# Performance work log

Measured on AMD Instinct MI355X. Metric: run time of the kernel, lower is better.

Reference implementation:

```python
import jax, jax.numpy as jnp
import numpy as np

E, T, A, H = 64, 128, 32, 4
S, O, QH1, QD, C1 = 256, 128, 128, 64, 128  # state, obs, query hidden, query/key dim, c hidden


def setup_inputs() -> dict:
    key = jax.random.key(0)
    ks = jax.random.split(key, 10)
    w = 0.02
    return {
        "q_values": jax.random.normal(ks[0], (E, T, A), jnp.float32),
        "states": jax.random.normal(ks[1], (E, T, S), jnp.float32),
        "individual_fs": jax.random.normal(ks[2], (E, T, A, O), jnp.float32),
        "Wq1": jax.random.normal(ks[3], (S, QH1), jnp.float32) * w,
        "bq1": jnp.zeros((QH1,), jnp.float32),
        "Wq2": jax.random.normal(ks[4], (QH1, QD), jnp.float32) * w,
        "bq2": jnp.zeros((QD,), jnp.float32),
        "Wk": jax.random.normal(ks[5], (H, O, QD), jnp.float32) * w,
        "bk": jnp.zeros((H, QD), jnp.float32),
        "Wc1": jax.random.normal(ks[6], (S, C1), jnp.float32) * w,
        "bc1": jnp.zeros((C1,), jnp.float32),
        "Wc2": jax.random.normal(ks[7], (C1, 1), jnp.float32) * w,
        "bc2": jnp.zeros((1,), jnp.float32),
    }


def reference(q_values, states, individual_fs, Wq1, bq1, Wq2, bq2, Wk, bk, Wc1, bc1, Wc2, bc2):
    e, t, a = q_values.shape
    s = states.reshape(-1, states.shape[-1])              # (B, S), B = E*T
    f = individual_fs.reshape(e * t, a, -1)               # (B, A, O)
    # query embedding of state: 2-layer MLP with ReLU
    emb_s = jnp.maximum(s @ Wq1 + bq1, 0.0) @ Wq2 + bq2   # (B, QD)
    # all-agents, all-heads key extraction in one batched einsum
    emb_u = jnp.einsum('bao,hok->bahk', f, Wk) + bk       # (B, A, H, QD)
    # query-key dot products per agent/head, then sum over heads
    Lambda_i = jnp.einsum('bk,bahk->bah', emb_s, emb_u).sum(axis=-1)  # (B, A)
    # state-dependent scalar bias
    c_value = jnp.maximum(s @ Wc1 + bc1, 0.0) @ Wc2 + bc2  # (B, 1)
    Q_tot = jnp.sum(Lambda_i * q_values.reshape(-1, a), axis=-1, keepdims=True) + c_value
    return Q_tot.reshape(e, t, 1)
```

## Files before the change

### kernel.cpp

```cpp
#include <hip/hip_runtime.h>


static constexpr int Sd  = 256;
static constexpr int Ad  = 32;
static constexpr int Od  = 128;
static constexpr int QDd = 64;
static constexpr int NB  = 8;

__global__ void qatten_prep(const float* __restrict__ Wk, const float* __restrict__ bk,
                            float* __restrict__ WkT, float* __restrict__ bkSum)
{
    int idx = blockIdx.x * 256 + threadIdx.x;
    int k = idx >> 7;
    int o = idx & 127;
    float s = 0.f;
#pragma unroll
    for (int h = 0; h < 4; ++h) s += Wk[h * (Od * QDd) + o * QDd + k];
    WkT[k * Od + o] = s;
    if (idx < QDd) {
        float t = 0.f;
#pragma unroll
        for (int h = 0; h < 4; ++h) t += bk[h * QDd + idx];
        bkSum[idx] = t;
    }
}

__global__ __launch_bounds__(256, 4) void qatten_fused(
    const float* __restrict__ qv, const float* __restrict__ st, const float* __restrict__ fs,
    const float* __restrict__ Wq1, const float* __restrict__ bq1,
    const float* __restrict__ Wq2, const float* __restrict__ bq2,
    const float* __restrict__ Wc1, const float* __restrict__ bc1,
    const float* __restrict__ Wc2, const float* __restrict__ bc2,
    const float* __restrict__ WkT, const float* __restrict__ bkSum,
    float* __restrict__ out)
{
    __shared__ float s_lds[NB][Sd];
    __shared__ float h_lds[NB][260];
    __shared__ float emb_lds[NB][QDd];
    __shared__ float v_lds[NB][Od];
    __shared__ float q_lds[NB][Ad];
    __shared__ float red_lds[NB][4];
    __shared__ float bias_lds[NB];

    const int tid = threadIdx.x;
    const int b0 = blockIdx.x * NB;

    {
        const float4* sp = (const float4*)(st + (size_t)b0 * Sd);
        float4* sl = (float4*)&s_lds[0][0];
        sl[tid] = sp[tid];
        sl[tid + 256] = sp[tid + 256];
        (&q_lds[0][0])[tid] = qv[(size_t)b0 * Ad + tid];
    }
    __syncthreads();

    {
        const float* W  = (tid < 128) ? (Wq1 + tid) : (Wc1 + (tid - 128));
        const float  bb = (tid < 128) ? bq1[tid] : bc1[tid - 128];
        float acc[NB];
#pragma unroll
        for (int r = 0; r < NB; ++r) acc[r] = 0.f;
#pragma unroll 4
        for (int i = 0; i < Sd; i += 4) {
            const float w0 = W[(size_t)(i + 0) * 128];
            const float w1 = W[(size_t)(i + 1) * 128];
            const float w2 = W[(size_t)(i + 2) * 128];
            const float w3 = W[(size_t)(i + 3) * 128];
#pragma unroll
            for (int r = 0; r < NB; ++r) {
                const float4 sv = *(const float4*)&s_lds[r][i];
                float a = acc[r];
                a = fmaf(sv.x, w0, a);
                a = fmaf(sv.y, w1, a);
                a = fmaf(sv.z, w2, a);
                a = fmaf(sv.w, w3, a);
                acc[r] = a;
            }
        }
#pragma unroll
        for (int r = 0; r < NB; ++r)
            h_lds[r][tid] = fmaxf(acc[r] + bb, 0.f);
    }
    __syncthreads();

    {
        const int k = tid & 63;
        const int rg = tid >> 6;
        float a0 = 0.f, a1 = 0.f;
#pragma unroll 4
        for (int j = 0; j < 128; j += 4) {
            const float w0 = Wq2[(size_t)(j + 0) * 64 + k];
            const float w1 = Wq2[(size_t)(j + 1) * 64 + k];
            const float w2 = Wq2[(size_t)(j + 2) * 64 + k];
            const float w3 = Wq2[(size_t)(j + 3) * 64 + k];
            const float4 h0 = *(const float4*)&h_lds[rg][j];
            const float4 h1 = *(const float4*)&h_lds[rg + 4][j];
            a0 = fmaf(h0.x, w0, a0);  a1 = fmaf(h1.x, w0, a1);
            a0 = fmaf(h0.y, w1, a0);  a1 = fmaf(h1.y, w1, a1);
            a0 = fmaf(h0.z, w2, a0);  a1 = fmaf(h1.z, w2, a1);
            a0 = fmaf(h0.w, w3, a0);  a1 = fmaf(h1.w, w3, a1);
        }
        const float bias = bq2[k];
        emb_lds[rg][k] = a0 + bias;
        emb_lds[rg + 4][k] = a1 + bias;
    }
    __syncthreads();

    {
        const int o = tid & 127;
        const int rg = (tid >> 7) * 4;
        float acc[4] = {0.f, 0.f, 0.f, 0.f};
#pragma unroll 4
        for (int k = 0; k < QDd; k += 4) {
            const float w0 = WkT[(size_t)(k + 0) * 128 + o];
            const float w1 = WkT[(size_t)(k + 1) * 128 + o];
            const float w2 = WkT[(size_t)(k + 2) * 128 + o];
            const float w3 = WkT[(size_t)(k + 3) * 128 + o];
#pragma unroll
            for (int r = 0; r < 4; ++r) {
                const float4 ev = *(const float4*)&emb_lds[rg + r][k];
                float a = acc[r];
                a = fmaf(ev.x, w0, a);
                a = fmaf(ev.y, w1, a);
                a = fmaf(ev.z, w2, a);
                a = fmaf(ev.w, w3, a);
                acc[r] = a;
            }
        }
#pragma unroll
        for (int r = 0; r < 4; ++r) v_lds[rg + r][o] = acc[r];
    }

    {
        const int b = tid >> 5;
        const int i = tid & 31;
        float pb = 0.f, pc = 0.f;
#pragma unroll
        for (int k = i; k < QDd; k += 32)  pb = fmaf(emb_lds[b][k], bkSum[k], pb);
#pragma unroll
        for (int j = i; j < 128; j += 32)  pc = fmaf(h_lds[b][128 + j], Wc2[j], pc);
        float pq = q_lds[b][i];
#pragma unroll
        for (int d = 16; d >= 1; d >>= 1) {
            pb += __shfl_down(pb, d, 32);
            pc += __shfl_down(pc, d, 32);
            pq += __shfl_down(pq, d, 32);
        }
        if (i == 0) bias_lds[b] = (pc + bc2[0]) + pb * pq;
    }
    __syncthreads();

    {
        const int oq = tid & 31;
        const int ag = tid >> 5;
        float acc[NB];
#pragma unroll
        for (int b = 0; b < NB; ++b) {
            const float4* fb = (const float4*)(fs + (size_t)(b0 + b) * (Ad * Od));
            const float4 v4 = *(const float4*)&v_lds[b][oq * 4];
            float s = 0.f;
#pragma unroll
            for (int r = 0; r < 4; ++r) {
                const int a = ag + 8 * r;
                const float4 f4 = fb[a * 32 + oq];
                float d = f4.x * v4.x;
                d = fmaf(f4.y, v4.y, d);
                d = fmaf(f4.z, v4.z, d);
                d = fmaf(f4.w, v4.w, d);
                s = fmaf(q_lds[b][a], d, s);
            }
            acc[b] = s;
        }
        const int lane = tid & 63;
        const int wv = tid >> 6;
#pragma unroll
        for (int b = 0; b < NB; ++b) {
            float s = acc[b];
#pragma unroll
            for (int d = 32; d >= 1; d >>= 1) s += __shfl_xor(s, d);
            acc[b] = s;
        }
        if (lane == 0) {
#pragma unroll
            for (int b = 0; b < NB; ++b) red_lds[b][wv] = acc[b];
        }
    }
    __syncthreads();

    if (tid < NB) {
        out[b0 + tid] = red_lds[tid][0] + red_lds[tid][1] +
                        red_lds[tid][2] + red_lds[tid][3] + bias_lds[tid];
    }
}

extern "C" void kernel_launch(void* const* d_in, const int* in_sizes, int n_in,
                              void* d_out, int out_size, void* d_ws, size_t ws_size,
                              hipStream_t stream) {
    const float* qv  = (const float*)d_in[0];
    const float* st  = (const float*)d_in[1];
    const float* fs  = (const float*)d_in[2];
    const float* Wq1 = (const float*)d_in[3];
    const float* bq1 = (const float*)d_in[4];
    const float* Wq2 = (const float*)d_in[5];
    const float* bq2 = (const float*)d_in[6];
    const float* Wk  = (const float*)d_in[7];
    const float* bk  = (const float*)d_in[8];
    const float* Wc1 = (const float*)d_in[9];
    const float* bc1 = (const float*)d_in[10];
    const float* Wc2 = (const float*)d_in[11];
    const float* bc2 = (const float*)d_in[12];
    float* out = (float*)d_out;

    float* WkT   = (float*)d_ws;
    float* bkSum = WkT + QDd * Od;

    qatten_prep<<<32, 256, 0, stream>>>(Wk, bk, WkT, bkSum);
    qatten_fused<<<1024, 256, 0, stream>>>(qv, st, fs, Wq1, bq1, Wq2, bq2,
                                           Wc1, bc1, Wc2, bc2, WkT, bkSum, out);
}
```

Baseline: 249.9 us.

## Split MLP and feature reduction into independent block roles with final combine

Reorders the computation so the large individual_fs stream is reduced against q_values (g = sum_a q_a f_a) in dedicated blocks that do not depend on the MLP. Separate blocks in the same launch compute the key-projected query vector v and the bias. A small final kernel takes the dot product of g and v. This decouples the memory-bound fs read from the serial MLP chain so the two can run concurrently on different CUs. In exchange it adds workspace round-trips for v and g and a third kernel launch.

```diff
diff --git a/kernel.cpp b/kernel.cpp
--- a/kernel.cpp
+++ b/kernel.cpp
@@ -6,6 +6,8 @@
 static constexpr int Od  = 128;
 static constexpr int QDd = 64;
 static constexpr int NB  = 8;
+static constexpr int A_BLOCKS = 1024;
+static constexpr int B_BLOCKS = 2048;
 
 __global__ void qatten_prep(const float* __restrict__ Wk, const float* __restrict__ bk,
                             float* __restrict__ WkT, float* __restrict__ bkSum)
@@ -25,172 +27,167 @@
     }
 }
 
-__global__ __launch_bounds__(256, 4) void qatten_fused(
+__global__ __launch_bounds__(256, 6) void qatten_main(
     const float* __restrict__ qv, const float* __restrict__ st, const float* __restrict__ fs,
     const float* __restrict__ Wq1, const float* __restrict__ bq1,
     const float* __restrict__ Wq2, const float* __restrict__ bq2,
     const float* __restrict__ Wc1, const float* __restrict__ bc1,
     const float* __restrict__ Wc2, const float* __restrict__ bc2,
     const float* __restrict__ WkT, const float* __restrict__ bkSum,
-    float* __restrict__ out)
+    float* __restrict__ v_out, float* __restrict__ bias_out, float* __restrict__ g_out)
 {
     __shared__ float s_lds[NB][Sd];
     __shared__ float h_lds[NB][260];
     __shared__ float emb_lds[NB][QDd];
-    __shared__ float v_lds[NB][Od];
-    __shared__ float q_lds[NB][Ad];
-    __shared__ float red_lds[NB][4];
-    __shared__ float bias_lds[NB];
 
     const int tid = threadIdx.x;
-    const int b0 = blockIdx.x * NB;
-
-    {
-        const float4* sp = (const float4*)(st + (size_t)b0 * Sd);
-        float4* sl = (float4*)&s_lds[0][0];
-        sl[tid] = sp[tid];
-        sl[tid + 256] = sp[tid + 256];
-        (&q_lds[0][0])[tid] = qv[(size_t)b0 * Ad + tid];
+
+    if (blockIdx.x < A_BLOCKS) {
+        const int b0 = blockIdx.x * NB;
+
+        {
+            const float4* sp = (const float4*)(st + (size_t)b0 * Sd);
+            float4* sl = (float4*)&s_lds[0][0];
+            sl[tid] = sp[tid];
+            sl[tid + 256] = sp[tid + 256];
+        }
+        __syncthreads();
+
+        {
+            const float* W  = (tid < 128) ? (Wq1 + tid) : (Wc1 + (tid - 128));
+            const float  bb = (tid < 128) ? bq1[tid] : bc1[tid - 128];
+            float acc[NB];
+#pragma unroll
+            for (int r = 0; r < NB; ++r) acc[r] = 0.f;
+#pragma unroll 4
+            for (int i = 0; i < Sd; i += 4) {
+                const float w0 = W[(size_t)(i + 0) * 128];
+                const float w1 = W[(size_t)(i + 1) * 128];
+                const float w2 = W[(size_t)(i + 2) * 128];
+                const float w3 = W[(size_t)(i + 3) * 128];
+#pragma unroll
+                for (int r = 0; r < NB; ++r) {
+                    const float4 sv = *(const float4*)&s_lds[r][i];
+                    float a = acc[r];
+                    a = fmaf(sv.x, w0, a);
+                    a = fmaf(sv.y, w1, a);
+                    a = fmaf(sv.z, w2, a);
+                    a = fmaf(sv.w, w3, a);
+                    acc[r] = a;
+                }
+            }
+#pragma unroll
+            for (int r = 0; r < NB; ++r)
+                h_lds[r][tid] = fmaxf(acc[r] + bb, 0.f);
+        }
+        __syncthreads();
+
+        {
+            const int k = tid & 63;
+            const int rg = tid >> 6;
+            float a0 = 0.f, a1 = 0.f;
+#pragma unroll 4
+            for (int j = 0; j < 128; j += 4) {
+                const float w0 = Wq2[(size_t)(j + 0) * 64 + k];
+                const float w1 = Wq2[(size_t)(j + 1) * 64 + k];
+                const float w2 = Wq2[(size_t)(j + 2) * 64 + k];
+                const float w3 = Wq2[(size_t)(j + 3) * 64 + k];
+                const float4 h0 = *(const float4*)&h_lds[rg][j];
+                const float4 h1 = *(const float4*)&h_lds[rg + 4][j];
+                a0 = fmaf(h0.x, w0, a0);  a1 = fmaf(h1.x, w0, a1);
+                a0 = fmaf(h0.y, w1, a0);  a1 = fmaf(h1.y, w1, a1);
+                a0 = fmaf(h0.z, w2, a0);  a1 = fmaf(h1.z, w2, a1);
+                a0 = fmaf(h0.w, w3, a0);  a1 = fmaf(h1.w, w3, a1);
+            }
+            const float bias = bq2[k];
+            emb_lds[rg][k] = a0 + bias;
+            emb_lds[rg + 4][k] = a1 + bias;
+        }
+        __syncthreads();
+
+        {
+            const int o = tid & 127;
+            const int rg = (tid >> 7) * 4;
+            float acc[4] = {0.f, 0.f, 0.f, 0.f};
+#pragma unroll 4
+            for (int k = 0; k < QDd; k += 4) {
+                const float w0 = WkT[(size_t)(k + 0) * 128 + o];
+                const float w1 = WkT[(size_t)(k + 1) * 128 + o];
+                const float w2 = WkT[(size_t)(k + 2) * 128 + o];
+                const float w3 = WkT[(size_t)(k + 3) * 128 + o];
+#pragma unroll
+                for (int r = 0; r < 4; ++r) {
+                    const float4 ev = *(const float4*)&emb_lds[rg + r][k];
+                    float a = acc[r];
+                    a = fmaf(ev.x, w0, a);
+                    a = fmaf(ev.y, w1, a);
+                    a = fmaf(ev.z, w2, a);
+                    a = fmaf(ev.w, w3, a);
+                    acc[r] = a;
+                }
+            }
+#pragma unroll
+            for (int r = 0; r < 4; ++r)
+                v_out[(size_t)(b0 + rg + r) * Od + o] = acc[r];
+        }
+
+        {
+            const int b = tid >> 5;
+            const int i = tid & 31;
+            float pb = 0.f, pc = 0.f;
+#pragma unroll
+            for (int k = i; k < QDd; k += 32)  pb = fmaf(emb_lds[b][k], bkSum[k], pb);
+#pragma unroll
+            for (int j = i; j < 128; j += 32)  pc = fmaf(h_lds[b][128 + j], Wc2[j], pc);
+            float pq = qv[(size_t)b0 * Ad + tid];
+#pragma unroll
+            for (int d = 16; d >= 1; d >>= 1) {
+                pb += __shfl_down(pb, d, 32);
+                pc += __shfl_down(pc, d, 32);
+                pq += __shfl_down(pq, d, 32);
+            }
+            if (i == 0) bias_out[b0 + b] = (pc + bc2[0]) + pb * pq;
+        }
+    } else {
+        const int bb = ((int)blockIdx.x - A_BLOCKS) * 4 + (tid >> 6);
+        const int l  = tid & 63;
+        const float4* __restrict__ fb = (const float4*)fs + (size_t)bb * (Ad * Od / 4);
+        const float qreg = qv[(size_t)bb * Ad + (l & 31)];
+        float4 acc = {0.f, 0.f, 0.f, 0.f};
+#pragma unroll
+        for (int i = 0; i < 16; ++i) {
+            const float4 f4 = fb[i * 64 + l];
+            const float  qa = __shfl(qreg, 2 * i + (l >> 5), 64);
+            acc.x = fmaf(qa, f4.x, acc.x);
+            acc.y = fmaf(qa, f4.y, acc.y);
+            acc.z = fmaf(qa, f4.z, acc.z);
+            acc.w = fmaf(qa, f4.w, acc.w);
+        }
+        acc.x += __shfl_xor(acc.x, 32, 64);
+        acc.y += __shfl_xor(acc.y, 32, 64);
+        acc.z += __shfl_xor(acc.z, 32, 64);
+        acc.w += __shfl_xor(acc.w, 32, 64);
+        if (l < 32)
+            *(float4*)(g_out + (size_t)bb * Od + l * 4) = acc;
     }
-    __syncthreads();
-
-    {
-        const float* W  = (tid < 128) ? (Wq1 + tid) : (Wc1 + (tid - 128));
-        const float  bb = (tid < 128) ? bq1[tid] : bc1[tid - 128];
-        float acc[NB];
-#pragma unroll
-        for (int r = 0; r < NB; ++r) acc[r] = 0.f;
-#pragma unroll 4
-        for (int i = 0; i < Sd; i += 4) {
-            const float w0 = W[(size_t)(i + 0) * 128];
-            const float w1 = W[(size_t)(i + 1) * 128];
-            const float w2 = W[(size_t)(i + 2) * 128];
-            const float w3 = W[(size_t)(i + 3) * 128];
-#pragma unroll
-            for (int r = 0; r < NB; ++r) {
-                const float4 sv = *(const float4*)&s_lds[r][i];
-                float a = acc[r];
-                a = fmaf(sv.x, w0, a);
-                a = fmaf(sv.y, w1, a);
-                a = fmaf(sv.z, w2, a);
-                a = fmaf(sv.w, w3, a);
-                acc[r] = a;
-            }
-        }
-#pragma unroll
-        for (int r = 0; r < NB; ++r)
-            h_lds[r][tid] = fmaxf(acc[r] + bb, 0.f);
-    }
-    __syncthreads();
-
-    {
-        const int k = tid & 63;
-        const int rg = tid >> 6;
-        float a0 = 0.f, a1 = 0.f;
-#pragma unroll 4
-        for (int j = 0; j < 128; j += 4) {
-            const float w0 = Wq2[(size_t)(j + 0) * 64 + k];
-            const float w1 = Wq2[(size_t)(j + 1) * 64 + k];
-            const float w2 = Wq2[(size_t)(j + 2) * 64 + k];
-            const float w3 = Wq2[(size_t)(j + 3) * 64 + k];
-            const float4 h0 = *(const float4*)&h_lds[rg][j];
-            const float4 h1 = *(const float4*)&h_lds[rg + 4][j];
-            a0 = fmaf(h0.x, w0, a0);  a1 = fmaf(h1.x, w0, a1);
-            a0 = fmaf(h0.y, w1, a0);  a1 = fmaf(h1.y, w1, a1);
-            a0 = fmaf(h0.z, w2, a0);  a1 = fmaf(h1.z, w2, a1);
-            a0 = fmaf(h0.w, w3, a0);  a1 = fmaf(h1.w, w3, a1);
-        }
-        const float bias = bq2[k];
-        emb_lds[rg][k] = a0 + bias;
-        emb_lds[rg + 4][k] = a1 + bias;
-    }
-    __syncthreads();
-
-    {
-        const int o = tid & 127;
-        const int rg = (tid >> 7) * 4;
-        float acc[4] = {0.f, 0.f, 0.f, 0.f};
-#pragma unroll 4
-        for (int k = 0; k < QDd; k += 4) {
-            const float w0 = WkT[(size_t)(k + 0) * 128 + o];
-            const float w1 = WkT[(size_t)(k + 1) * 128 + o];
-            const float w2 = WkT[(size_t)(k + 2) * 128 + o];
-            const float w3 = WkT[(size_t)(k + 3) * 128 + o];
-#pragma unroll
-            for (int r = 0; r < 4; ++r) {
-                const float4 ev = *(const float4*)&emb_lds[rg + r][k];
-                float a = acc[r];
-                a = fmaf(ev.x, w0, a);
-                a = fmaf(ev.y, w1, a);
-                a = fmaf(ev.z, w2, a);
-                a = fmaf(ev.w, w3, a);
-                acc[r] = a;
-            }
-        }
-#pragma unroll
-        for (int r = 0; r < 4; ++r) v_lds[rg + r][o] = acc[r];
-    }
-
-    {
-        const int b = tid >> 5;
-        const int i = tid & 31;
-        float pb = 0.f, pc = 0.f;
-#pragma unroll
-        for (int k = i; k < QDd; k += 32)  pb = fmaf(emb_lds[b][k], bkSum[k], pb);
-#pragma unroll
-        for (int j = i; j < 128; j += 32)  pc = fmaf(h_lds[b][128 + j], Wc2[j], pc);
-        float pq = q_lds[b][i];
-#pragma unroll
-        for (int d = 16; d >= 1; d >>= 1) {
-            pb += __shfl_down(pb, d, 32);
-            pc += __shfl_down(pc, d, 32);
-            pq += __shfl_down(pq, d, 32);
-        }
-        if (i == 0) bias_lds[b] = (pc + bc2[0]) + pb * pq;
-    }
-    __syncthreads();
-
-    {
-        const int oq = tid & 31;
-        const int ag = tid >> 5;
-        float acc[NB];
-#pragma unroll
-        for (int b = 0; b < NB; ++b) {
-            const float4* fb = (const float4*)(fs + (size_t)(b0 + b) * (Ad * Od));
-            const float4 v4 = *(const float4*)&v_lds[b][oq * 4];
-            float s = 0.f;
-#pragma unroll
-            for (int r = 0; r < 4; ++r) {
-                const int a = ag + 8 * r;
-                const float4 f4 = fb[a * 32 + oq];
-                float d = f4.x * v4.x;
-                d = fmaf(f4.y, v4.y, d);
-                d = fmaf(f4.z, v4.z, d);
-                d = fmaf(f4.w, v4.w, d);
-                s = fmaf(q_lds[b][a], d, s);
-            }
-            acc[b] = s;
-        }
-        const int lane = tid & 63;
-        const int wv = tid >> 6;
-#pragma unroll
-        for (int b = 0; b < NB; ++b) {
-            float s = acc[b];
-#pragma unroll
-            for (int d = 32; d >= 1; d >>= 1) s += __shfl_xor(s, d);
-            acc[b] = s;
-        }
-        if (lane == 0) {
-#pragma unroll
-            for (int b = 0; b < NB; ++b) red_lds[b][wv] = acc[b];
-        }
-    }
-    __syncthreads();
-
-    if (tid < NB) {
-        out[b0 + tid] = red_lds[tid][0] + red_lds[tid][1] +
-                        red_lds[tid][2] + red_lds[tid][3] + bias_lds[tid];
-    }
+}
+
+__global__ __launch_bounds__(256, 8) void qatten_final(
+    const float* __restrict__ g, const float* __restrict__ v,
+    const float* __restrict__ bias, float* __restrict__ out)
+{
+    const int tid = threadIdx.x;
+    const int b = blockIdx.x * 8 + (tid >> 5);
+    const int i = tid & 31;
+    const float4 gv = *(const float4*)(g + (size_t)b * Od + i * 4);
+    const float4 vv = *(const float4*)(v + (size_t)b * Od + i * 4);
+    float d = gv.x * vv.x;
+    d = fmaf(gv.y, vv.y, d);
+    d = fmaf(gv.z, vv.z, d);
+    d = fmaf(gv.w, vv.w, d);
+#pragma unroll
+    for (int k = 16; k >= 1; k >>= 1) d += __shfl_down(d, k, 32);
+    if (i == 0) out[b] = d + bias[b];
 }
 
 extern "C" void kernel_launch(void* const* d_in, const int* in_sizes, int n_in,
@@ -213,8 +210,13 @@
 
     float* WkT   = (float*)d_ws;
     float* bkSum = WkT + QDd * Od;
+    float* bias  = bkSum + QDd;
+    float* vbuf  = bias + 8192;
+    float* gbuf  = vbuf + 8192 * Od;
 
     qatten_prep<<<32, 256, 0, stream>>>(Wk, bk, WkT, bkSum);
-    qatten_fused<<<1024, 256, 0, stream>>>(qv, st, fs, Wq1, bq1, Wq2, bq2,
-                                           Wc1, bc1, Wc2, bc2, WkT, bkSum, out);
-}
+    qatten_main<<<A_BLOCKS + B_BLOCKS, 256, 0, stream>>>(
+        qv, st, fs, Wq1, bq1, Wq2, bq2, Wc1, bc1, Wc2, bc2,
+        WkT, bkSum, vbuf, bias, gbuf);
+    qatten_final<<<1024, 256, 0, stream>>>(gbuf, vbuf, bias, out);
+}
```

Measured after the change: 256.5 us. 2.7% more time.
